# Kernel optimization log

Hardware: AMD Instinct MI355X
Metric: run time of the kernel (lower is better)

## Reference

```python
import jax, jax.numpy as jnp
import numpy as np

N = 100000      # nodes
E = 1600000     # edges (before self-loops)
F_DIM = 256     # feat_dim
H = 64          # hidden_dim
EPS = 1e-5      # BatchNorm eps
NEG_SLOPE = 0.2 # PyG GATConv leaky_relu slope


def _glorot(key, shape):
    fan_in, fan_out = shape[0], shape[-1]
    s = jnp.sqrt(2.0 / (fan_in + fan_out)).astype(jnp.float32)
    return jax.random.normal(key, shape, dtype=jnp.float32) * s


def setup_inputs() -> dict:
    key = jax.random.key(0)
    ks = jax.random.split(key, 16)
    inp = {
        "feat": jax.random.normal(ks[0], (N, F_DIM), dtype=jnp.float32),
        "edge_index": jax.random.randint(ks[1], (2, E), 0, N, dtype=jnp.int64)
        if jax.config.jax_enable_x64 else jax.random.randint(ks[1], (2, E), 0, N).astype(jnp.int32),
    }
    dims = [(F_DIM, H), (H, H), (H, H), (H, F_DIM)]  # gc1-enc, gc2-enc, gc1-dec, gc2-dec
    for i, (din, dout) in enumerate(dims, start=1):
        k = jax.random.split(ks[1 + i], 4)
        inp[f"W{i}"] = _glorot(k[0], (din, dout))
        inp[f"as{i}"] = _glorot(k[1], (dout,))
        inp[f"ad{i}"] = _glorot(k[2], (dout,))
        inp[f"bi{i}"] = jnp.zeros((dout,), dtype=jnp.float32)
    # BatchNorm affine params (eval mode: running_mean=0, running_var=1)
    for i in range(1, 4):
        inp[f"g{i}"] = jnp.ones((H,), dtype=jnp.float32)
        inp[f"be{i}"] = jnp.zeros((H,), dtype=jnp.float32)
    return inp


def _gat(x, src, dst, W, a_src, a_dst, b, n):
    # PyG single-head GATConv: h = xW; e_ij = LeakyReLU(a_s.h_i + a_d.h_j);
    # alpha = softmax over edges sharing a destination; out_j = sum alpha_ij h_i + b
    h = x @ W                                   # [N, dout]
    e = jax.nn.leaky_relu((h @ a_src)[src] + (h @ a_dst)[dst], NEG_SLOPE)  # [Etot]
    m = jax.ops.segment_max(e, dst, num_segments=n)
    m = jnp.where(jnp.isfinite(m), m, 0.0)
    p = jnp.exp(e - m[dst])
    denom = jax.ops.segment_sum(p, dst, num_segments=n)
    alpha = p / (denom[dst] + 1e-16)
    out = jax.ops.segment_sum(alpha[:, None] * h[src], dst, num_segments=n)
    return out + b


def _bn_eval(x, gamma, beta):
    # eval-mode BatchNorm1d with running_mean=0, running_var=1
    return x * (gamma / jnp.sqrt(1.0 + EPS)) + beta


def reference(feat, edge_index,
              W1, as1, ad1, bi1, W2, as2, ad2, bi2,
              W3, as3, ad3, bi3, W4, as4, ad4, bi4,
              g1, be1, g2, be2, g3, be3):
    n = feat.shape[0]
    loops = jnp.arange(n, dtype=edge_index.dtype)
    src = jnp.concatenate([edge_index[0], loops])  # add_self_loops=True
    dst = jnp.concatenate([edge_index[1], loops])
    # GraphEncoder
    x = jax.nn.relu(_gat(feat, src, dst, W1, as1, ad1, bi1, n))
    x = _bn_eval(x, g1, be1)  # dropout inactive (eval)
    x = jax.nn.relu(_gat(x, src, dst, W2, as2, ad2, bi2, n))
    x = _bn_eval(x, g2, be2)
    # AttributeDecoder
    x = jax.nn.relu(_gat(x, src, dst, W3, as3, ad3, bi3, n))
    x = _bn_eval(x, g3, be3)
    x = jax.nn.relu(_gat(x, src, dst, W4, as4, ad4, bi4, n))
    return x
```

## Files before the change

kernel.cpp:

```cpp
#include <hip/hip_runtime.h>
#include <cmath>

#define SLOPE 0.2f
#define EPSV 1e-5f

__global__ __launch_bounds__(256) void deg_init_kernel(int* __restrict__ deg, int n) {
    int i = blockIdx.x * 256 + threadIdx.x;
    if (i <= n) deg[i] = (i < n) ? 1 : 0;
}

__global__ __launch_bounds__(256) void hist_kernel(const int* __restrict__ dst, int E,
                                                   int* __restrict__ deg) {
    int stride = gridDim.x * 256;
    for (int e = blockIdx.x * 256 + threadIdx.x; e < E; e += stride)
        atomicAdd(&deg[dst[e]], 1);
}

__global__ __launch_bounds__(256) void scan_block_kernel(const int* __restrict__ deg,
                                                         int* __restrict__ row,
                                                         int* __restrict__ partials, int n1) {
    __shared__ int s[256];
    int t = threadIdx.x;
    int i = blockIdx.x * 256 + t;
    int v = (i < n1) ? deg[i] : 0;
    s[t] = v;
    __syncthreads();
    for (int off = 1; off < 256; off <<= 1) {
        int x = (t >= off) ? s[t - off] : 0;
        __syncthreads();
        s[t] += x;
        __syncthreads();
    }
    if (i < n1) row[i] = s[t] - v;
    if (t == 255) partials[blockIdx.x] = s[255];
}

__global__ __launch_bounds__(1024) void scan_top_kernel(int* __restrict__ partials, int nb) {
    __shared__ int s[1024];
    int t = threadIdx.x;
    int v = (t < nb) ? partials[t] : 0;
    s[t] = v;
    __syncthreads();
    for (int off = 1; off < 1024; off <<= 1) {
        int x = (t >= off) ? s[t - off] : 0;
        __syncthreads();
        s[t] += x;
        __syncthreads();
    }
    if (t < nb) partials[t] = s[t] - v;
}

__global__ __launch_bounds__(256) void scan_add_kernel(int* __restrict__ row,
                                                       const int* __restrict__ partials, int n1) {
    int i = blockIdx.x * 256 + threadIdx.x;
    if (i < n1) row[i] += partials[blockIdx.x];
}

__global__ __launch_bounds__(256) void fill_self_kernel(const int* __restrict__ row,
                                                        int* __restrict__ cursor,
                                                        int* __restrict__ csr, int n) {
    int i = blockIdx.x * 256 + threadIdx.x;
    if (i < n) {
        int p = row[i];
        csr[p] = i;
        cursor[i] = p + 1;
    }
}

__global__ __launch_bounds__(256) void fill_edge_kernel(const int* __restrict__ src,
                                                        const int* __restrict__ dst, int E,
                                                        int* __restrict__ cursor,
                                                        int* __restrict__ csr) {
    int stride = gridDim.x * 256;
    for (int e = blockIdx.x * 256 + threadIdx.x; e < E; e += stride) {
        int p = atomicAdd(&cursor[dst[e]], 1);
        csr[p] = src[e];
    }
}

template <int KTILES>
__global__ __launch_bounds__(64, 4) void gemm_scores_kernel(
    const float* __restrict__ X, const float* __restrict__ W,
    const float* __restrict__ a_s, const float* __restrict__ a_d,
    float* __restrict__ H, float* __restrict__ s_src, float* __restrict__ s_dst,
    int n) {
    const int lane = threadIdx.x;
    const int base = blockIdx.x * 16;
    if (base >= n) return;

    float acc[16];
#pragma unroll
    for (int g = 0; g < 16; ++g) acc[g] = 0.f;

#pragma unroll 1
    for (int t = 0; t < KTILES; ++t) {
        float wcol[64];
#pragma unroll
        for (int k = 0; k < 64; ++k) wcol[k] = W[(t * 64 + k) * 64 + lane];
#pragma unroll
        for (int g = 0; g < 16; ++g) {
            const int node = base + g;
            if (node < n) {
                const float4* xr = reinterpret_cast<const float4*>(
                    X + (size_t)node * (KTILES * 64) + t * 64);
#pragma unroll
                for (int k4 = 0; k4 < 16; ++k4) {
                    float4 x4 = xr[k4];
                    acc[g] = fmaf(x4.x, wcol[4 * k4 + 0],
                             fmaf(x4.y, wcol[4 * k4 + 1],
                             fmaf(x4.z, wcol[4 * k4 + 2],
                             fmaf(x4.w, wcol[4 * k4 + 3], acc[g]))));
                }
            }
        }
    }

    const float as_l = a_s[lane], ad_l = a_d[lane];
#pragma unroll
    for (int g = 0; g < 16; ++g) {
        const int node = base + g;
        if (node >= n) break;
        float h = acc[g];
        H[(size_t)node * 64 + lane] = h;
        float ps = h * as_l, pd = h * ad_l;
#pragma unroll
        for (int off = 32; off; off >>= 1) {
            ps += __shfl_xor(ps, off);
            pd += __shfl_xor(pd, off);
        }
        if (lane == 0) {
            s_src[node] = ps;
            s_dst[node] = pd;
        }
    }
}

__global__ __launch_bounds__(256) void scores_x_kernel(
    const float* __restrict__ X, const float* __restrict__ Was,
    const float* __restrict__ Wad, float* __restrict__ s_src,
    float* __restrict__ s_dst, int n) {
    const int lane = threadIdx.x & 63;
    const int node = (blockIdx.x * 256 + threadIdx.x) >> 6;
    if (node >= n) return;
    float x = X[(size_t)node * 64 + lane];
    float ps = x * Was[lane];
    float pd = x * Wad[lane];
#pragma unroll
    for (int off = 32; off; off >>= 1) {
        ps += __shfl_xor(ps, off);
        pd += __shfl_xor(pd, off);
    }
    if (lane == 0) {
        s_src[node] = ps;
        s_dst[node] = pd;
    }
}

__global__ __launch_bounds__(128) void wa_kernel(const float* __restrict__ W ,
                                                 const float* __restrict__ a_s,
                                                 const float* __restrict__ a_d,
                                                 float* __restrict__ Was,
                                                 float* __restrict__ Wad) {
    int t = threadIdx.x;
    int k = t & 63;
    const float* a = (t < 64) ? a_s : a_d;
    float* o = (t < 64) ? Was : Wad;
    const float4* wr = reinterpret_cast<const float4*>(W + (size_t)k * 256);
    const float4* a4 = reinterpret_cast<const float4*>(a);
    float acc = 0.f;
#pragma unroll
    for (int j = 0; j < 64; ++j) {
        float4 w = wr[j];
        float4 av = a4[j];
        acc = fmaf(w.x, av.x, acc);
        acc = fmaf(w.y, av.y, acc);
        acc = fmaf(w.z, av.z, acc);
        acc = fmaf(w.w, av.w, acc);
    }
    o[k] = acc;
}

template <int MODE>
__global__ __launch_bounds__(256) void gather_kernel(
    const int* __restrict__ row, const int* __restrict__ csr,
    const float* __restrict__ s_src, const float* __restrict__ s_dst,
    const float* __restrict__ H, const float* __restrict__ bi,
    const float* __restrict__ g, const float* __restrict__ be,
    float* __restrict__ Out, int n) {
    const int lane = threadIdx.x & 63;
    const int node = (blockIdx.x * 256 + threadIdx.x) >> 6;
    if (node >= n) return;
    const int beg = row[node];
    const int end = row[node + 1];
    const int deg = end - beg;
    const float sdd = s_dst[node];

    const int e0 = beg + lane;
    int c0 = 0;
    float v0 = -1e30f;
    bool has0 = (e0 < end);
    if (has0) {
        c0 = csr[e0];
        float t = s_src[c0] + sdd;
        v0 = t >= 0.f ? t : SLOPE * t;
    }
    float m = v0;
    float dl = has0 ? 1.f : 0.f;
    for (int e = e0 + 64; e < end; e += 64) {
        int s = csr[e];
        float t = s_src[s] + sdd;
        t = t >= 0.f ? t : SLOPE * t;
        float nm = fmaxf(m, t);
        dl = dl * __expf(m - nm) + __expf(t - nm);
        m = nm;
    }
    float M = m;
#pragma unroll
    for (int off = 32; off; off >>= 1) M = fmaxf(M, __shfl_xor(M, off));
    dl *= __expf(m - M);
#pragma unroll
    for (int off = 32; off; off >>= 1) dl += __shfl_xor(dl, off);
    const float invden = 1.f / (dl + 1e-16f);
    const float p0 = has0 ? __expf(v0 - M) : 0.f;

    float acc = 0.f;
    const int nf = deg < 64 ? deg : 64;
    int k = 0;
    for (; k + 8 <= nf; k += 8) {
        int s0 = __shfl(c0, k + 0), s1 = __shfl(c0, k + 1);
        int s2 = __shfl(c0, k + 2), s3 = __shfl(c0, k + 3);
        int s4 = __shfl(c0, k + 4), s5 = __shfl(c0, k + 5);
        int s6 = __shfl(c0, k + 6), s7 = __shfl(c0, k + 7);
        float a0 = __shfl(p0, k + 0), a1 = __shfl(p0, k + 1);
        float a2 = __shfl(p0, k + 2), a3 = __shfl(p0, k + 3);
        float a4 = __shfl(p0, k + 4), a5 = __shfl(p0, k + 5);
        float a6 = __shfl(p0, k + 6), a7 = __shfl(p0, k + 7);
        float h0 = H[(size_t)s0 * 64 + lane], h1 = H[(size_t)s1 * 64 + lane];
        float h2 = H[(size_t)s2 * 64 + lane], h3 = H[(size_t)s3 * 64 + lane];
        float h4 = H[(size_t)s4 * 64 + lane], h5 = H[(size_t)s5 * 64 + lane];
        float h6 = H[(size_t)s6 * 64 + lane], h7 = H[(size_t)s7 * 64 + lane];
        acc = fmaf(a0, h0, acc); acc = fmaf(a1, h1, acc);
        acc = fmaf(a2, h2, acc); acc = fmaf(a3, h3, acc);
        acc = fmaf(a4, h4, acc); acc = fmaf(a5, h5, acc);
        acc = fmaf(a6, h6, acc); acc = fmaf(a7, h7, acc);
    }
    for (; k < nf; ++k) {
        int s = __shfl(c0, k);
        float a = __shfl(p0, k);
        acc = fmaf(a, H[(size_t)s * 64 + lane], acc);
    }
    for (int e = beg + 64; e < end; ++e) {
        int s = csr[e];
        float t = s_src[s] + sdd;
        t = t >= 0.f ? t : SLOPE * t;
        acc = fmaf(__expf(t - M), H[(size_t)s * 64 + lane], acc);
    }
    acc *= invden;

    float o;
    if (MODE == 0) {
        o = fmaxf(acc + bi[lane], 0.f) * (g[lane] * rsqrtf(1.f + EPSV)) + be[lane];
    } else {
        o = acc;
    }
    Out[(size_t)node * 64 + lane] = o;
}

__global__ __launch_bounds__(64, 4) void gemm_out_kernel(const float* __restrict__ X,
                                                         const float* __restrict__ W,
                                                         const float* __restrict__ bi,
                                                         float* __restrict__ Out, int n) {
    const int lane = threadIdx.x;
    const int base = blockIdx.x * 16;
    if (base >= n) return;
#pragma unroll 1
    for (int q = 0; q < 4; ++q) {
        float wcol[64];
#pragma unroll
        for (int k = 0; k < 64; ++k) wcol[k] = W[k * 256 + q * 64 + lane];
        const float bj = bi[q * 64 + lane];
#pragma unroll
        for (int g = 0; g < 16; ++g) {
            const int node = base + g;
            if (node >= n) break;
            const float4* xr = reinterpret_cast<const float4*>(X + (size_t)node * 64);
            float acc = 0.f;
#pragma unroll
            for (int k4 = 0; k4 < 16; ++k4) {
                float4 x4 = xr[k4];
                acc = fmaf(x4.x, wcol[4 * k4 + 0],
                      fmaf(x4.y, wcol[4 * k4 + 1],
                      fmaf(x4.z, wcol[4 * k4 + 2],
                      fmaf(x4.w, wcol[4 * k4 + 3], acc))));
            }
            Out[(size_t)node * 256 + q * 64 + lane] = fmaxf(acc + bj, 0.f);
        }
    }
}

extern "C" void kernel_launch(void* const* d_in, const int* in_sizes, int n_in,
                              void* d_out, int out_size, void* d_ws,
                              size_t ws_size, hipStream_t stream) {
    const float* feat = (const float*)d_in[0];
    const int* eidx = (const int*)d_in[1];
    const float* W[4] = {(const float*)d_in[2], (const float*)d_in[6],
                         (const float*)d_in[10], (const float*)d_in[14]};
    const float* As[4] = {(const float*)d_in[3], (const float*)d_in[7],
                          (const float*)d_in[11], (const float*)d_in[15]};
    const float* Ad[4] = {(const float*)d_in[4], (const float*)d_in[8],
                          (const float*)d_in[12], (const float*)d_in[16]};
    const float* Bi[4] = {(const float*)d_in[5], (const float*)d_in[9],
                          (const float*)d_in[13], (const float*)d_in[17]};
    const float* G[3] = {(const float*)d_in[18], (const float*)d_in[20],
                         (const float*)d_in[22]};
    const float* Be[3] = {(const float*)d_in[19], (const float*)d_in[21],
                          (const float*)d_in[23]};

    const int N = in_sizes[0] / 256;
    const int E = in_sizes[1] / 2;
    const int* srcA = eidx;
    const int* dstA = eidx + E;

    float* h = (float*)d_ws;
    float* xA = h + (size_t)N * 64;
    float* xB = xA + (size_t)N * 64;
    float* s_src = xB + (size_t)N * 64;
    float* s_dst = s_src + N;
    float* Was = s_dst + N;
    float* Wad = Was + 64;
    int* deg = (int*)(Wad + 64);
    int* row = deg + (N + 1);
    int* cursor = row + (N + 1);
    int* partials = cursor + N;
    int* csr = partials + 1024;

    const int n1 = N + 1;
    const int NB1 = (n1 + 255) / 256;
    const int node_grid = (N + 3) / 4;
    const int gemm_grid = (N + 15) / 16;
    (void)ws_size; (void)n_in; (void)out_size;

    deg_init_kernel<<<NB1, 256, 0, stream>>>(deg, N);
    hist_kernel<<<2048, 256, 0, stream>>>(dstA, E, deg);
    scan_block_kernel<<<NB1, 256, 0, stream>>>(deg, row, partials, n1);
    scan_top_kernel<<<1, 1024, 0, stream>>>(partials, NB1);
    scan_add_kernel<<<NB1, 256, 0, stream>>>(row, partials, n1);
    fill_self_kernel<<<NB1, 256, 0, stream>>>(row, cursor, csr, N);
    fill_edge_kernel<<<2048, 256, 0, stream>>>(srcA, dstA, E, cursor, csr);

    gemm_scores_kernel<4><<<gemm_grid, 64, 0, stream>>>(
        feat, W[0], As[0], Ad[0], h, s_src, s_dst, N);
    gather_kernel<0><<<node_grid, 256, 0, stream>>>(
        row, csr, s_src, s_dst, h, Bi[0], G[0], Be[0], xA, N);

    gemm_scores_kernel<1><<<gemm_grid, 64, 0, stream>>>(
        xA, W[1], As[1], Ad[1], h, s_src, s_dst, N);
    gather_kernel<0><<<node_grid, 256, 0, stream>>>(
        row, csr, s_src, s_dst, h, Bi[1], G[1], Be[1], xB, N);

    gemm_scores_kernel<1><<<gemm_grid, 64, 0, stream>>>(
        xB, W[2], As[2], Ad[2], h, s_src, s_dst, N);
    gather_kernel<0><<<node_grid, 256, 0, stream>>>(
        row, csr, s_src, s_dst, h, Bi[2], G[2], Be[2], xA, N);

    wa_kernel<<<1, 128, 0, stream>>>(W[3], As[3], Ad[3], Was, Wad);
    scores_x_kernel<<<node_grid, 256, 0, stream>>>(xA, Was, Wad, s_src, s_dst, N);
    gather_kernel<1><<<node_grid, 256, 0, stream>>>(
        row, csr, s_src, s_dst, xA, nullptr, nullptr, nullptr, h, N);
    gemm_out_kernel<<<gemm_grid, 64, 0, stream>>>(h, W[3], Bi[3], (float*)d_out, N);
}
```

Baseline: 1.205 ms.

## Stage weight tiles in LDS and use 4-wave blocks for dense GEMMs

The projection and output GEMM kernels now run 256-thread blocks. Each block cooperatively loads a 64x64 weight tile into shared memory, and each wave handles 4 nodes with 4 independent accumulators. Previously every 64-thread block reloaded the 64-element weight column into registers from global memory and processed 16 nodes serially. The change cuts redundant weight loads and register pressure and adds instruction-level parallelism, at the cost of block-wide barriers and LDS reads in the inner loop.

```diff
diff --git a/kernel.cpp b/kernel.cpp
--- a/kernel.cpp
+++ b/kernel.cpp
@@ -79,48 +79,76 @@
 }
 
 template <int KTILES>
-__global__ __launch_bounds__(64, 4) void gemm_scores_kernel(
+__global__ __launch_bounds__(256) void gemm_scores_kernel(
     const float* __restrict__ X, const float* __restrict__ W,
     const float* __restrict__ a_s, const float* __restrict__ a_d,
     float* __restrict__ H, float* __restrict__ s_src, float* __restrict__ s_dst,
     int n) {
-    const int lane = threadIdx.x;
-    const int base = blockIdx.x * 16;
-    if (base >= n) return;
-
-    float acc[16];
-#pragma unroll
-    for (int g = 0; g < 16; ++g) acc[g] = 0.f;
-
-#pragma unroll 1
+    __shared__ float Ws[64 * 64];
+    const int lane = threadIdx.x & 63;
+    const int wv = threadIdx.x >> 6;
+    const int base = blockIdx.x * 16 + wv * 4;
+    const bool full = (base + 4 <= n);
+
+    float acc0 = 0.f, acc1 = 0.f, acc2 = 0.f, acc3 = 0.f;
+
     for (int t = 0; t < KTILES; ++t) {
-        float wcol[64];
-#pragma unroll
-        for (int k = 0; k < 64; ++k) wcol[k] = W[(t * 64 + k) * 64 + lane];
-#pragma unroll
-        for (int g = 0; g < 16; ++g) {
-            const int node = base + g;
-            if (node < n) {
-                const float4* xr = reinterpret_cast<const float4*>(
-                    X + (size_t)node * (KTILES * 64) + t * 64);
+        if (t) __syncthreads();
+        {
+            const float4* W4 = reinterpret_cast<const float4*>(W + t * 4096);
+            float4* Ws4 = reinterpret_cast<float4*>(Ws);
+#pragma unroll
+            for (int i = 0; i < 4; ++i) Ws4[threadIdx.x + 256 * i] = W4[threadIdx.x + 256 * i];
+        }
+        __syncthreads();
+
+        if (full) {
+            const float4* x0 = reinterpret_cast<const float4*>(X + (size_t)(base + 0) * (KTILES * 64) + t * 64);
+            const float4* x1 = reinterpret_cast<const float4*>(X + (size_t)(base + 1) * (KTILES * 64) + t * 64);
+            const float4* x2 = reinterpret_cast<const float4*>(X + (size_t)(base + 2) * (KTILES * 64) + t * 64);
+            const float4* x3 = reinterpret_cast<const float4*>(X + (size_t)(base + 3) * (KTILES * 64) + t * 64);
+#pragma unroll
+            for (int k4 = 0; k4 < 16; ++k4) {
+                float4 xa = x0[k4], xb = x1[k4], xc = x2[k4], xd = x3[k4];
+                float w0 = Ws[(4 * k4 + 0) * 64 + lane];
+                float w1 = Ws[(4 * k4 + 1) * 64 + lane];
+                float w2 = Ws[(4 * k4 + 2) * 64 + lane];
+                float w3 = Ws[(4 * k4 + 3) * 64 + lane];
+                acc0 = fmaf(xa.x, w0, fmaf(xa.y, w1, fmaf(xa.z, w2, fmaf(xa.w, w3, acc0))));
+                acc1 = fmaf(xb.x, w0, fmaf(xb.y, w1, fmaf(xb.z, w2, fmaf(xb.w, w3, acc1))));
+                acc2 = fmaf(xc.x, w0, fmaf(xc.y, w1, fmaf(xc.z, w2, fmaf(xc.w, w3, acc2))));
+                acc3 = fmaf(xd.x, w0, fmaf(xd.y, w1, fmaf(xd.z, w2, fmaf(xd.w, w3, acc3))));
+            }
+        } else if (base < n) {
+            for (int g = 0; g < 4; ++g) {
+                const int node = base + g;
+                if (node >= n) break;
+                const float4* xr = reinterpret_cast<const float4*>(X + (size_t)node * (KTILES * 64) + t * 64);
+                float a = 0.f;
 #pragma unroll
                 for (int k4 = 0; k4 < 16; ++k4) {
                     float4 x4 = xr[k4];
-                    acc[g] = fmaf(x4.x, wcol[4 * k4 + 0],
-                             fmaf(x4.y, wcol[4 * k4 + 1],
-                             fmaf(x4.z, wcol[4 * k4 + 2],
-                             fmaf(x4.w, wcol[4 * k4 + 3], acc[g]))));
+                    a = fmaf(x4.x, Ws[(4 * k4 + 0) * 64 + lane],
+                        fmaf(x4.y, Ws[(4 * k4 + 1) * 64 + lane],
+                        fmaf(x4.z, Ws[(4 * k4 + 2) * 64 + lane],
+                        fmaf(x4.w, Ws[(4 * k4 + 3) * 64 + lane], a))));
                 }
+                if (g == 0) acc0 += a;
+                else if (g == 1) acc1 += a;
+                else if (g == 2) acc2 += a;
+                else acc3 += a;
             }
         }
     }
 
+    if (base >= n) return;
     const float as_l = a_s[lane], ad_l = a_d[lane];
-#pragma unroll
-    for (int g = 0; g < 16; ++g) {
+    float accs[4] = {acc0, acc1, acc2, acc3};
+#pragma unroll
+    for (int g = 0; g < 4; ++g) {
         const int node = base + g;
         if (node >= n) break;
-        float h = acc[g];
+        float h = accs[g];
         H[(size_t)node * 64 + lane] = h;
         float ps = h * as_l, pd = h * ad_l;
 #pragma unroll
@@ -266,34 +294,68 @@
     Out[(size_t)node * 64 + lane] = o;
 }
 
-__global__ __launch_bounds__(64, 4) void gemm_out_kernel(const float* __restrict__ X,
-                                                         const float* __restrict__ W,
-                                                         const float* __restrict__ bi,
-                                                         float* __restrict__ Out, int n) {
-    const int lane = threadIdx.x;
-    const int base = blockIdx.x * 16;
-    if (base >= n) return;
-#pragma unroll 1
+__global__ __launch_bounds__(256) void gemm_out_kernel(const float* __restrict__ X,
+                                                       const float* __restrict__ W,
+                                                       const float* __restrict__ bi,
+                                                       float* __restrict__ Out, int n) {
+    __shared__ float Ws[64 * 64];
+    const int lane = threadIdx.x & 63;
+    const int wv = threadIdx.x >> 6;
+    const int base = blockIdx.x * 16 + wv * 4;
+    const bool full = (base + 4 <= n);
+
     for (int q = 0; q < 4; ++q) {
-        float wcol[64];
-#pragma unroll
-        for (int k = 0; k < 64; ++k) wcol[k] = W[k * 256 + q * 64 + lane];
+        if (q) __syncthreads();
+        {
+            float4* Ws4 = reinterpret_cast<float4*>(Ws);
+#pragma unroll
+            for (int i = 0; i < 4; ++i) {
+                int idx = threadIdx.x + 256 * i;
+                int r = idx >> 4, c4 = idx & 15;
+                Ws4[idx] = reinterpret_cast<const float4*>(W + (size_t)r * 256 + q * 64)[c4];
+            }
+        }
+        __syncthreads();
+        if (base >= n) continue;
         const float bj = bi[q * 64 + lane];
-#pragma unroll
-        for (int g = 0; g < 16; ++g) {
-            const int node = base + g;
-            if (node >= n) break;
-            const float4* xr = reinterpret_cast<const float4*>(X + (size_t)node * 64);
-            float acc = 0.f;
+        if (full) {
+            const float4* x0 = reinterpret_cast<const float4*>(X + (size_t)(base + 0) * 64);
+            const float4* x1 = reinterpret_cast<const float4*>(X + (size_t)(base + 1) * 64);
+            const float4* x2 = reinterpret_cast<const float4*>(X + (size_t)(base + 2) * 64);
+            const float4* x3 = reinterpret_cast<const float4*>(X + (size_t)(base + 3) * 64);
+            float acc0 = 0.f, acc1 = 0.f, acc2 = 0.f, acc3 = 0.f;
 #pragma unroll
             for (int k4 = 0; k4 < 16; ++k4) {
-                float4 x4 = xr[k4];
-                acc = fmaf(x4.x, wcol[4 * k4 + 0],
-                      fmaf(x4.y, wcol[4 * k4 + 1],
-                      fmaf(x4.z, wcol[4 * k4 + 2],
-                      fmaf(x4.w, wcol[4 * k4 + 3], acc))));
+                float4 xa = x0[k4], xb = x1[k4], xc = x2[k4], xd = x3[k4];
+                float w0 = Ws[(4 * k4 + 0) * 64 + lane];
+                float w1 = Ws[(4 * k4 + 1) * 64 + lane];
+                float w2 = Ws[(4 * k4 + 2) * 64 + lane];
+                float w3 = Ws[(4 * k4 + 3) * 64 + lane];
+                acc0 = fmaf(xa.x, w0, fmaf(xa.y, w1, fmaf(xa.z, w2, fmaf(xa.w, w3, acc0))));
+                acc1 = fmaf(xb.x, w0, fmaf(xb.y, w1, fmaf(xb.z, w2, fmaf(xb.w, w3, acc1))));
+                acc2 = fmaf(xc.x, w0, fmaf(xc.y, w1, fmaf(xc.z, w2, fmaf(xc.w, w3, acc2))));
+                acc3 = fmaf(xd.x, w0, fmaf(xd.y, w1, fmaf(xd.z, w2, fmaf(xd.w, w3, acc3))));
             }
-            Out[(size_t)node * 256 + q * 64 + lane] = fmaxf(acc + bj, 0.f);
+            Out[(size_t)(base + 0) * 256 + q * 64 + lane] = fmaxf(acc0 + bj, 0.f);
+            Out[(size_t)(base + 1) * 256 + q * 64 + lane] = fmaxf(acc1 + bj, 0.f);
+            Out[(size_t)(base + 2) * 256 + q * 64 + lane] = fmaxf(acc2 + bj, 0.f);
+            Out[(size_t)(base + 3) * 256 + q * 64 + lane] = fmaxf(acc3 + bj, 0.f);
+        } else {
+            for (int g = 0; g < 4; ++g) {
+                const int node = base + g;
+                if (node >= n) break;
+                const float4* xr = reinterpret_cast<const float4*>(X + (size_t)node * 64);
+                float a = 0.f;
+#pragma unroll
+                for (int k4 = 0; k4 < 16; ++k4) {
+                    float4 x4 = xr[k4];
+                    a = fmaf(x4.x, Ws[(4 * k4 + 0) * 64 + lane],
+                        fmaf(x4.y, Ws[(4 * k4 + 1) * 64 + lane],
+                        fmaf(x4.z, Ws[(4 * k4 + 2) * 64 + lane],
+                        fmaf(x4.w, Ws[(4 * k4 + 3) * 64 + lane], a))));
+                }
+                Out[(size_t)node * 256 + q * 64 + lane] = fmaxf(a + bj, 0.f);
+            }
         }
     }
 }
@@ -348,17 +410,17 @@
     fill_self_kernel<<<NB1, 256, 0, stream>>>(row, cursor, csr, N);
     fill_edge_kernel<<<2048, 256, 0, stream>>>(srcA, dstA, E, cursor, csr);
 
-    gemm_scores_kernel<4><<<gemm_grid, 64, 0, stream>>>(
+    gemm_scores_kernel<4><<<gemm_grid, 256, 0, stream>>>(
         feat, W[0], As[0], Ad[0], h, s_src, s_dst, N);
     gather_kernel<0><<<node_grid, 256, 0, stream>>>(
         row, csr, s_src, s_dst, h, Bi[0], G[0], Be[0], xA, N);
 
-    gemm_scores_kernel<1><<<gemm_grid, 64, 0, stream>>>(
+    gemm_scores_kernel<1><<<gemm_grid, 256, 0, stream>>>(
         xA, W[1], As[1], Ad[1], h, s_src, s_dst, N);
     gather_kernel<0><<<node_grid, 256, 0, stream>>>(
         row, csr, s_src, s_dst, h, Bi[1], G[1], Be[1], xB, N);
 
-    gemm_scores_kernel<1><<<gemm_grid, 64, 0, stream>>>(
+    gemm_scores_kernel<1><<<gemm_grid, 256, 0, stream>>>(
         xB, W[2], As[2], Ad[2], h, s_src, s_dst, N);
     gather_kernel<0><<<node_grid, 256, 0, stream>>>(
         row, csr, s_src, s_dst, h, Bi[2], G[2], Be[2], xA, N);
@@ -367,5 +429,5 @@
     scores_x_kernel<<<node_grid, 256, 0, stream>>>(xA, Was, Wad, s_src, s_dst, N);
     gather_kernel<1><<<node_grid, 256, 0, stream>>>(
         row, csr, s_src, s_dst, xA, nullptr, nullptr, nullptr, h, N);
-    gemm_out_kernel<<<gemm_grid, 64, 0, stream>>>(h, W[3], Bi[3], (float*)d_out, N);
-}
+    gemm_out_kernel<<<gemm_grid, 256, 0, stream>>>(h, W[3], Bi[3], (float*)d_out, N);
+}
```

Measured after the change: 1.196 ms. No clear change (-0.8%).
